# Kernel tuning notes

Hardware: AMD Instinct MI355X
Metric: run time of the kernel (lower is better)

Reference implementation:

```python
import jax, jax.numpy as jnp
import numpy as np

N_HEAD, MODEL_DIM, KEY_DIM, VALUE_DIM = 16, 1024, 64, 64
B, S = 4, 2048
EPS = 1e-5
TEMP = float(np.sqrt(KEY_DIM))


def setup_inputs() -> dict:
    key = jax.random.key(0)
    ks = jax.random.split(key, 12)
    d = {
        'query': jax.random.normal(ks[0], (B, S, MODEL_DIM), jnp.float32),
        'key':   jax.random.normal(ks[1], (B, S, MODEL_DIM), jnp.float32),
        'value': jax.random.normal(ks[2], (B, S, MODEL_DIM), jnp.float32),
        # projection weights stored as [in, out]
        'Wq': jax.random.normal(ks[3], (MODEL_DIM, N_HEAD * KEY_DIM), jnp.float32) * np.sqrt(2.0 / (MODEL_DIM + KEY_DIM)),
        'bq': jnp.zeros((N_HEAD * KEY_DIM,), jnp.float32),
        'Wk': jax.random.normal(ks[4], (MODEL_DIM, N_HEAD * KEY_DIM), jnp.float32) * np.sqrt(2.0 / (MODEL_DIM + KEY_DIM)),
        'bk': jnp.zeros((N_HEAD * KEY_DIM,), jnp.float32),
        'Wv': jax.random.normal(ks[5], (MODEL_DIM, N_HEAD * VALUE_DIM), jnp.float32) * np.sqrt(2.0 / (MODEL_DIM + VALUE_DIM)),
        'bv': jnp.zeros((N_HEAD * VALUE_DIM,), jnp.float32),
        'Wo': jax.random.normal(ks[6], (N_HEAD * VALUE_DIM, MODEL_DIM), jnp.float32) * np.sqrt(2.0 / (N_HEAD * VALUE_DIM + MODEL_DIM)),
        'bo': jnp.zeros((MODEL_DIM,), jnp.float32),
        'ln_gamma': jnp.ones((MODEL_DIM,), jnp.float32),
        'ln_beta': jnp.zeros((MODEL_DIM,), jnp.float32),
    }
    return d


def reference(query, key, value, Wq, bq, Wk, bk, Wv, bv, Wo, bo, ln_gamma, ln_beta):
    b, sq, _ = query.shape
    residual = query
    # QKV projections -> [B, S, H, D]
    q = (query @ Wq + bq).reshape(b, sq, N_HEAD, KEY_DIM)
    k = (key @ Wk + bk).reshape(b, key.shape[1], N_HEAD, KEY_DIM)
    v = (value @ Wv + bv).reshape(b, value.shape[1], N_HEAD, VALUE_DIM)
    # scaled dot-product attention (dropout inactive in eval)
    scores = jnp.einsum('bqhd,bkhd->bhqk', q, k) / TEMP
    attn = jax.nn.softmax(scores, axis=-1)
    out = jnp.einsum('bhqk,bkhd->bqhd', attn, v).reshape(b, sq, N_HEAD * VALUE_DIM)
    # output projection + residual + LayerNorm
    out = out @ Wo + bo + residual
    mu = jnp.mean(out, axis=-1, keepdims=True)
    var = jnp.var(out, axis=-1, keepdims=True)
    return (out - mu) * jax.lax.rsqrt(var + EPS) * ln_gamma + ln_beta
```

## Files before the change

### kernel.cpp

```cpp
#include <hip/hip_runtime.h>
#include <math.h>

#define MD 1024
#define NH 16
#define HD 64
#define BATCH 4
#define SEQ 2048

typedef __attribute__((ext_vector_type(8))) short short8;
typedef __attribute__((ext_vector_type(4))) short short4v;
typedef __attribute__((ext_vector_type(4))) float f32x4;
typedef __attribute__((ext_vector_type(2))) unsigned int uint2v;

#define GLOAD16(gp, lp) __builtin_amdgcn_global_load_lds( \
    (const __attribute__((address_space(1))) void*)(gp),  \
    (__attribute__((address_space(3))) void*)(lp), 16, 0, 0)

__device__ inline unsigned short f2b(float f) {
    unsigned u = __builtin_bit_cast(unsigned, f);
    unsigned r = (u + 0x7fffu + ((u >> 16) & 1u)) >> 16;
    return (unsigned short)r;
}
__device__ inline float b2f(unsigned short s) {
    return __builtin_bit_cast(float, ((unsigned)s) << 16);
}

__global__ __launch_bounds__(256)
void prep_kernel(const float* __restrict__ x0, const float* __restrict__ x1,
                 const float* __restrict__ x2, unsigned short* __restrict__ y0,
                 unsigned short* __restrict__ y1, unsigned short* __restrict__ y2,
                 int n,
                 const float* __restrict__ W0, const float* __restrict__ W1,
                 const float* __restrict__ W2, const float* __restrict__ W3,
                 unsigned short* __restrict__ T0, unsigned short* __restrict__ T1,
                 unsigned short* __restrict__ T2, unsigned short* __restrict__ T3)
{
    __shared__ __attribute__((aligned(16))) float T[64][68];
    const int tid = threadIdx.x;
    if (blockIdx.y < 3) {
        const float* x = (blockIdx.y == 0) ? x0 : (blockIdx.y == 1) ? x1 : x2;
        unsigned short* y = (blockIdx.y == 0) ? y0 : (blockIdx.y == 1) ? y1 : y2;
        int i = (blockIdx.x * 256 + tid) * 8;
        if (i >= n) return;
        f32x4 a = *(const f32x4*)(x + i);
        f32x4 b = *(const f32x4*)(x + i + 4);
        short8 o;
        o[0] = (short)f2b(a[0]); o[1] = (short)f2b(a[1]);
        o[2] = (short)f2b(a[2]); o[3] = (short)f2b(a[3]);
        o[4] = (short)f2b(b[0]); o[5] = (short)f2b(b[1]);
        o[6] = (short)f2b(b[2]); o[7] = (short)f2b(b[3]);
        *(short8*)(y + i) = o;
        return;
    }
    const int bx = blockIdx.x;
    if (bx >= 1024) return;
    const int z = bx >> 8, t = bx & 255;
    const int nt = t & 15, kt = t >> 4;
    const float* W = (z == 0) ? W0 : (z == 1) ? W1 : (z == 2) ? W2 : W3;
    unsigned short* WT = (z == 0) ? T0 : (z == 1) ? T1 : (z == 2) ? T2 : T3;
    #pragma unroll
    for (int i = 0; i < 4; ++i) {
        int u = tid + i * 256;
        int row = u >> 4, c4 = u & 15;
        f32x4 v = *(const f32x4*)(W + (size_t)(kt * 64 + row) * MD + nt * 64 + c4 * 4);
        *(f32x4*)&T[row][c4 * 4] = v;
    }
    __syncthreads();
    #pragma unroll
    for (int i = 0; i < 2; ++i) {
        int u = tid + i * 256;
        int nn = u >> 3, c16 = u & 7;
        short8 o;
        #pragma unroll
        for (int j = 0; j < 8; ++j) o[j] = (short)f2b(T[c16 * 8 + j][nn]);
        *(short8*)(WT + (size_t)(nt * 64 + nn) * MD + kt * 64 + c16 * 8) = o;
    }
}

__global__ __launch_bounds__(256)
void vtrans(const unsigned short* __restrict__ vp, unsigned short* __restrict__ vt)
{
    __shared__ __attribute__((aligned(16))) short T[64][72];
    const int tid = threadIdx.x;
    const int st = blockIdx.x, bh = blockIdx.y;
    const int b = bh >> 4, h = bh & 15;
    #pragma unroll
    for (int i = 0; i < 2; ++i) {
        int u = tid + i * 256;
        int row = u >> 3, c16 = u & 7;
        short8 v = *(const short8*)(vp + ((size_t)b * SEQ + st * 64 + row) * MD + h * 64 + c16 * 8);
        *(short8*)&T[row][c16 * 8] = v;
    }
    __syncthreads();
    #pragma unroll
    for (int i = 0; i < 2; ++i) {
        int u = tid + i * 256;
        int d = u >> 3, c16 = u & 7;
        short8 o;
        #pragma unroll
        for (int j = 0; j < 8; ++j) o[j] = T[c16 * 8 + j][d];
        *(short8*)(vt + ((size_t)bh * 64 + d) * SEQ + st * 64 + c16 * 8) = o;
    }
}

__device__ __forceinline__
void gemm_body(const unsigned short* __restrict__ A,
               const unsigned short* __restrict__ Bt,
               const float* __restrict__ bias,
               const float* __restrict__ residual,
               unsigned short* __restrict__ Cb,
               float* __restrict__ Cf,
               short* As, short* Bs)
{
    const int tid = threadIdx.x;
    const int lane = tid & 63;
    const int wave = tid >> 6;
    const int wm = wave >> 1, wn = wave & 1;
    const int l15 = lane & 15, g = lane >> 4;

    const int nbx = gridDim.x;
    const int bid = blockIdx.y * nbx + blockIdx.x;
    const int cpx = (nbx * gridDim.y) >> 3;
    const int swz = (bid & 7) * cpx + (bid >> 3);
    const int brow = (swz / nbx) * 128;
    const int bcol = (swz % nbx) * 128;

    f32x4 acc[4][4];
    #pragma unroll
    for (int m = 0; m < 4; ++m)
        #pragma unroll
        for (int n = 0; n < 4; ++n) acc[m][n] = (f32x4){0.f, 0.f, 0.f, 0.f};

    for (int k0 = 0; k0 < MD; k0 += 64) {
        __syncthreads();
        #pragma unroll
        for (int i = 0; i < 4; ++i) {
            const int U = (i * 4 + wave) * 64 + lane;
            const int row = U >> 3, c16 = U & 7;
            GLOAD16(A  + (size_t)(brow + row) * MD + k0 + c16 * 8, &As[U * 8]);
            GLOAD16(Bt + (size_t)(bcol + row) * MD + k0 + c16 * 8, &Bs[U * 8]);
        }
        __syncthreads();
        #pragma unroll
        for (int kk = 0; kk < 64; kk += 32) {
            short8 af[4], bf_[4];
            #pragma unroll
            for (int m = 0; m < 4; ++m)
                af[m] = *(const short8*)&As[(wm * 64 + m * 16 + l15) * 64 + kk + g * 8];
            #pragma unroll
            for (int n = 0; n < 4; ++n)
                bf_[n] = *(const short8*)&Bs[(wn * 64 + n * 16 + l15) * 64 + kk + g * 8];
            #pragma unroll
            for (int m = 0; m < 4; ++m)
                #pragma unroll
                for (int n = 0; n < 4; ++n)
                    acc[m][n] = __builtin_amdgcn_mfma_f32_16x16x32_bf16(af[m], bf_[n], acc[m][n], 0, 0, 0);
        }
    }

    #pragma unroll
    for (int m = 0; m < 4; ++m) {
        #pragma unroll
        for (int n = 0; n < 4; ++n) {
            const int col = bcol + wn * 64 + n * 16 + l15;
            const float bcol_v = bias[col];
            #pragma unroll
            for (int r = 0; r < 4; ++r) {
                const size_t row = (size_t)(brow + wm * 64 + m * 16 + 4 * g + r);
                float v = acc[m][n][r] + bcol_v;
                if (residual) v += residual[row * MD + col];
                if (Cb) Cb[row * MD + col] = f2b(v);
                else    Cf[row * MD + col] = v;
            }
        }
    }
}

__global__ __launch_bounds__(256, 2)
void gemm_qkv(const unsigned short* __restrict__ A0, const unsigned short* __restrict__ A1,
              const unsigned short* __restrict__ A2,
              const unsigned short* __restrict__ B0, const unsigned short* __restrict__ B1,
              const unsigned short* __restrict__ B2,
              const float* __restrict__ b0, const float* __restrict__ b1,
              const float* __restrict__ b2,
              unsigned short* __restrict__ C0, unsigned short* __restrict__ C1,
              unsigned short* __restrict__ C2)
{
    __shared__ __attribute__((aligned(16))) short As[128 * 64];
    __shared__ __attribute__((aligned(16))) short Bs[128 * 64];
    const int z = blockIdx.z;
    const unsigned short* A  = (z == 0) ? A0 : (z == 1) ? A1 : A2;
    const unsigned short* Bt = (z == 0) ? B0 : (z == 1) ? B1 : B2;
    const float* bias        = (z == 0) ? b0 : (z == 1) ? b1 : b2;
    unsigned short* C        = (z == 0) ? C0 : (z == 1) ? C1 : C2;
    gemm_body(A, Bt, bias, nullptr, C, nullptr, As, Bs);
}

__global__ __launch_bounds__(256, 2)
void gemm_o(const unsigned short* __restrict__ A, const unsigned short* __restrict__ Bt,
            const float* __restrict__ bias, const float* __restrict__ residual,
            float* __restrict__ Cf)
{
    __shared__ __attribute__((aligned(16))) short As[128 * 64];
    __shared__ __attribute__((aligned(16))) short Bs[128 * 64];
    gemm_body(A, Bt, bias, residual, nullptr, Cf, As, Bs);
}

__global__ __launch_bounds__(256, 2)
void attn_mfma(const unsigned short* __restrict__ qp,
               const unsigned short* __restrict__ kp,
               const unsigned short* __restrict__ vt,
               unsigned short* __restrict__ ao)
{
    __shared__ __attribute__((aligned(16))) short QPs[128 * 64];
    __shared__ __attribute__((aligned(16))) short Ks[2][64 * 64];
    __shared__ __attribute__((aligned(16))) short Vts[2][64 * 64];

    const int tid = threadIdx.x;
    const int lane = tid & 63;
    const int wave = tid >> 6;
    const int l15 = lane & 15, g = lane >> 4;
    const int qt = blockIdx.x, bh = blockIdx.y;
    const int b = bh >> 4, h = bh & 15;
    const size_t rowbase = (size_t)b * SEQ;
    const int q0 = qt * 128;
    const int wq = wave * 32;
    const int NT = SEQ / 64;

    const int r0 = tid >> 3, c16 = tid & 7;
    const int r1 = (tid + 256) >> 3;
    const int lds0 = (r0 * 8 + (c16 ^ (r0 & 7))) * 8;
    const int lds1 = (r1 * 8 + (c16 ^ (r1 & 7))) * 8;
    const unsigned short* kbase = kp + (rowbase + r0) * MD + h * 64 + c16 * 8;
    const unsigned short* vbase = vt + ((size_t)bh * 64 + r0) * SEQ + c16 * 8;

    const float qscale = 0.125f * 1.44269504088896f;
    #pragma unroll
    for (int i = 0; i < 4; ++i) {
        int u = tid + i * 256;
        int row = u >> 3, cc = u & 7;
        short8 v = *(const short8*)(qp + (rowbase + q0 + row) * MD + h * 64 + cc * 8);
        short8 o;
        #pragma unroll
        for (int j = 0; j < 8; ++j)
            o[j] = (short)f2b(b2f((unsigned short)v[j]) * qscale);
        *(short8*)&QPs[(row * 8 + (cc ^ (row & 7))) * 8] = o;
    }

    {
        short8 k0v = *(const short8*)(kbase);
        short8 k1v = *(const short8*)(kbase + 32 * MD);
        short8 v0v = *(const short8*)(vbase);
        short8 v1v = *(const short8*)(vbase + 32 * SEQ);
        *(short8*)&Ks[0][lds0]  = k0v;
        *(short8*)&Ks[0][lds1]  = k1v;
        *(short8*)&Vts[0][lds0] = v0v;
        *(short8*)&Vts[0][lds1] = v1v;
    }
    __syncthreads();

    short8 qreg[2][2];
    #pragma unroll
    for (int nf = 0; nf < 2; ++nf)
        #pragma unroll
        for (int ki = 0; ki < 2; ++ki) {
            int row = wq + nf * 16 + l15;
            int cu = ki * 4 + g;
            qreg[nf][ki] = *(const short8*)&QPs[(row * 8 + (cu ^ (row & 7))) * 8];
        }

    short8 ones;
    #pragma unroll
    for (int j = 0; j < 8; ++j) ones[j] = (short)0x3F80;

    float mrun[2] = {-INFINITY, -INFINITY};
    f32x4 lrun[2];
    f32x4 off[2][4];
    #pragma unroll
    for (int qf = 0; qf < 2; ++qf) {
        lrun[qf] = (f32x4){0.f, 0.f, 0.f, 0.f};
        #pragma unroll
        for (int df = 0; df < 4; ++df) off[qf][df] = (f32x4){0.f, 0.f, 0.f, 0.f};
    }

    for (int kt = 0; kt < NT; ++kt) {
        const int cur = kt & 1;

        short8 kreg0, kreg1, vreg0, vreg1;
        if (kt + 1 < NT) {
            const unsigned short* kb = kbase + (size_t)(kt + 1) * 64 * MD;
            const unsigned short* vb = vbase + (kt + 1) * 64;
            kreg0 = *(const short8*)(kb);
            kreg1 = *(const short8*)(kb + 32 * MD);
            vreg0 = *(const short8*)(vb);
            vreg1 = *(const short8*)(vb + 32 * SEQ);
        }

        f32x4 sc[4][2];
        #pragma unroll
        for (int mf = 0; mf < 4; ++mf)
            #pragma unroll
            for (int nf = 0; nf < 2; ++nf) sc[mf][nf] = (f32x4){0.f, 0.f, 0.f, 0.f};
        __builtin_amdgcn_s_setprio(1);
        #pragma unroll
        for (int ki = 0; ki < 2; ++ki) {
            const int cu = ki * 4 + g;
            short8 af[4];
            #pragma unroll
            for (int mf = 0; mf < 4; ++mf) {
                int row = mf * 16 + l15;
                af[mf] = *(const short8*)&Ks[cur][(row * 8 + (cu ^ (row & 7))) * 8];
            }
            #pragma unroll
            for (int mf = 0; mf < 4; ++mf)
                #pragma unroll
                for (int nf = 0; nf < 2; ++nf)
                    sc[mf][nf] = __builtin_amdgcn_mfma_f32_16x16x32_bf16(af[mf], qreg[nf][ki], sc[mf][nf], 0, 0, 0);
        }
        __builtin_amdgcn_s_setprio(0);

        float pmax[2];
        #pragma unroll
        for (int nf = 0; nf < 2; ++nf) {
            float pm = -INFINITY;
            #pragma unroll
            for (int mf = 0; mf < 4; ++mf)
                #pragma unroll
                for (int r = 0; r < 4; ++r) pm = fmaxf(pm, sc[mf][nf][r]);
            pm = fmaxf(pm, __shfl_xor(pm, 16));
            pm = fmaxf(pm, __shfl_xor(pm, 32));
            pmax[nf] = pm;
        }
        const int defer = (pmax[0] <= mrun[0] + 8.0f) && (pmax[1] <= mrun[1] + 8.0f);
        if (!__all(defer)) {
            float corr[2];
            #pragma unroll
            for (int nf = 0; nf < 2; ++nf) {
                float mnew = fmaxf(mrun[nf], pmax[nf]);
                corr[nf] = __builtin_amdgcn_exp2f(mrun[nf] - mnew);
                mrun[nf] = mnew;
            }
            #pragma unroll
            for (int qf = 0; qf < 2; ++qf)
                #pragma unroll
                for (int r = 0; r < 4; ++r) {
                    float c = __shfl(corr[qf], 4 * g + r);
                    lrun[qf][r] *= c;
                    #pragma unroll
                    for (int df = 0; df < 4; ++df) off[qf][df][r] *= c;
                }
        }
        #pragma unroll
        for (int nf = 0; nf < 2; ++nf) {
            const float nm = mrun[nf];
            #pragma unroll
            for (int mf = 0; mf < 4; ++mf)
                #pragma unroll
                for (int r = 0; r < 4; ++r)
                    sc[mf][nf][r] = __builtin_amdgcn_exp2f(sc[mf][nf][r] - nm);
        }

        #pragma unroll
        for (int nf = 0; nf < 2; ++nf) {
            int row = wq + nf * 16 + l15;
            #pragma unroll
            for (int mf = 0; mf < 4; ++mf) {
                unsigned p01, p23;
                asm("v_cvt_pk_bf16_f32 %0, %1, %2" : "=v"(p01) : "v"(sc[mf][nf][0]), "v"(sc[mf][nf][1]));
                asm("v_cvt_pk_bf16_f32 %0, %1, %2" : "=v"(p23) : "v"(sc[mf][nf][2]), "v"(sc[mf][nf][3]));
                uint2v pk = {p01, p23};
                int su = (mf * 2 + (g >> 1)) ^ (row & 7);
                *(uint2v*)&QPs[row * 64 + su * 8 + (g & 1) * 4] = pk;
            }
        }

        f32x4 ts[2];
        ts[0] = (f32x4){0.f, 0.f, 0.f, 0.f};
        ts[1] = (f32x4){0.f, 0.f, 0.f, 0.f};
        __builtin_amdgcn_s_setprio(1);
        #pragma unroll
        for (int ki = 0; ki < 2; ++ki) {
            const int cu = ki * 4 + g;
            short8 pa[2], vb[4];
            #pragma unroll
            for (int qf = 0; qf < 2; ++qf) {
                int row = wq + qf * 16 + l15;
                pa[qf] = *(const short8*)&QPs[(row * 8 + (cu ^ (row & 7))) * 8];
            }
            #pragma unroll
            for (int df = 0; df < 4; ++df) {
                int d = df * 16 + l15;
                vb[df] = *(const short8*)&Vts[cur][(d * 8 + (cu ^ (d & 7))) * 8];
            }
            #pragma unroll
            for (int qf = 0; qf < 2; ++qf)
                #pragma unroll
                for (int df = 0; df < 4; ++df)
                    off[qf][df] = __builtin_amdgcn_mfma_f32_16x16x32_bf16(pa[qf], vb[df], off[qf][df], 0, 0, 0);
            #pragma unroll
            for (int qf = 0; qf < 2; ++qf)
                ts[qf] = __builtin_amdgcn_mfma_f32_16x16x32_bf16(pa[qf], ones, ts[qf], 0, 0, 0);
        }
        __builtin_amdgcn_s_setprio(0);
        #pragma unroll
        for (int qf = 0; qf < 2; ++qf)
            #pragma unroll
            for (int r = 0; r < 4; ++r) lrun[qf][r] += ts[qf][r];

        if (kt + 1 < NT) {
            const int nxt = cur ^ 1;
            *(short8*)&Ks[nxt][lds0]  = kreg0;
            *(short8*)&Ks[nxt][lds1]  = kreg1;
            *(short8*)&Vts[nxt][lds0] = vreg0;
            *(short8*)&Vts[nxt][lds1] = vreg1;
        }
        __syncthreads();
    }

    #pragma unroll
    for (int qf = 0; qf < 2; ++qf) {
        #pragma unroll
        for (int r = 0; r < 4; ++r) {
            const float inv = 1.0f / lrun[qf][r];
            const size_t row = rowbase + q0 + wq + qf * 16 + 4 * g + r;
            #pragma unroll
            for (int df = 0; df < 4; ++df) {
                float val = off[qf][df][r] * inv;
                ao[row * MD + h * 64 + df * 16 + l15] = f2b(val);
            }
        }
    }
}

__global__ __launch_bounds__(256)
void ln_kernel(float* __restrict__ X, const float* __restrict__ gamma,
               const float* __restrict__ beta)
{
    const int row = blockIdx.x;
    const int tid = threadIdx.x;
    float* px = X + (size_t)row * MD;
    f32x4 x = ((const f32x4*)px)[tid];
    float s  = x[0] + x[1] + x[2] + x[3];
    float ss = fmaf(x[0], x[0], fmaf(x[1], x[1], fmaf(x[2], x[2], x[3] * x[3])));
    #pragma unroll
    for (int off = 1; off < 64; off <<= 1) {
        s  += __shfl_xor(s,  off);
        ss += __shfl_xor(ss, off);
    }
    __shared__ float red[8];
    const int wid = tid >> 6;
    if ((tid & 63) == 0) { red[wid] = s; red[wid + 4] = ss; }
    __syncthreads();
    s  = red[0] + red[1] + red[2] + red[3];
    ss = red[4] + red[5] + red[6] + red[7];
    const float mu   = s * (1.0f / MD);
    const float var  = ss * (1.0f / MD) - mu * mu;
    const float rstd = rsqrtf(var + 1e-5f);
    f32x4 gm = ((const f32x4*)gamma)[tid];
    f32x4 be = ((const f32x4*)beta)[tid];
    f32x4 r;
    r[0] = (x[0] - mu) * rstd * gm[0] + be[0];
    r[1] = (x[1] - mu) * rstd * gm[1] + be[1];
    r[2] = (x[2] - mu) * rstd * gm[2] + be[2];
    r[3] = (x[3] - mu) * rstd * gm[3] + be[3];
    ((f32x4*)px)[tid] = r;
}

extern "C" void kernel_launch(void* const* d_in, const int* in_sizes, int n_in,
                              void* d_out, int out_size, void* d_ws, size_t ws_size,
                              hipStream_t stream)
{
    const float* query = (const float*)d_in[0];
    const float* key   = (const float*)d_in[1];
    const float* value = (const float*)d_in[2];
    const float* Wq = (const float*)d_in[3];
    const float* bq = (const float*)d_in[4];
    const float* Wk = (const float*)d_in[5];
    const float* bk = (const float*)d_in[6];
    const float* Wv = (const float*)d_in[7];
    const float* bv = (const float*)d_in[8];
    const float* Wo = (const float*)d_in[9];
    const float* bo = (const float*)d_in[10];
    const float* gamma = (const float*)d_in[11];
    const float* beta  = (const float*)d_in[12];
    float* out = (float*)d_out;

    const size_t NTOK = (size_t)BATCH * SEQ;
    const size_t ACT  = NTOK * MD;

    unsigned short* qa  = (unsigned short*)d_ws;
    unsigned short* ka  = qa + ACT;
    unsigned short* va  = ka + ACT;
    unsigned short* WqT = va + ACT;
    unsigned short* WkT = WqT + (size_t)MD * MD;
    unsigned short* WvT = WkT + (size_t)MD * MD;
    unsigned short* WoT = WvT + (size_t)MD * MD;
    unsigned short* qp  = WoT + (size_t)MD * MD;
    unsigned short* kp  = qp + ACT;
    unsigned short* vp  = kp + ACT;
    unsigned short* vtb = qa;
    unsigned short* ao  = ka;

    dim3 blk(256);

    prep_kernel<<<dim3(4096, 4), blk, 0, stream>>>(
        query, key, value, qa, ka, va, (int)ACT,
        Wq, Wk, Wv, Wo, WqT, WkT, WvT, WoT);

    dim3 gg(MD / 128, NTOK / 128, 3);
    gemm_qkv<<<gg, blk, 0, stream>>>(qa, ka, va, WqT, WkT, WvT,
                                     bq, bk, bv, qp, kp, vp);

    vtrans<<<dim3(SEQ / 64, 64), blk, 0, stream>>>(vp, vtb);

    attn_mfma<<<dim3(SEQ / 128, 64), blk, 0, stream>>>(qp, kp, vtb, ao);

    gemm_o<<<dim3(MD / 128, NTOK / 128), blk, 0, stream>>>(ao, WoT, bo, query, out);

    ln_kernel<<<NTOK, blk, 0, stream>>>(out, gamma, beta);
}
```

Measured before the change: 248.9 us.

## Fuse V transpose and Q scaling into QKV GEMM epilogue; widen attention tiles

The QKV GEMM epilogue now writes V directly in transposed per-head layout, which removes the separate vtrans kernel. It also folds the softmax scale (1/sqrt(d)·log2e) into Q, so attention loads Q fragments straight from global memory into registers instead of staging them through LDS. The attention kernel now processes 256 queries per block (64 per wave), doubling K/V reuse and halving the grid. The trade-off is higher register pressure (more accumulators and score tiles), a larger P buffer in LDS, and only 512 attention blocks, which may lower occupancy.

```diff
diff --git a/kernel.cpp b/kernel.cpp
--- a/kernel.cpp
+++ b/kernel.cpp
@@ -77,40 +77,11 @@
     }
 }
 
-__global__ __launch_bounds__(256)
-void vtrans(const unsigned short* __restrict__ vp, unsigned short* __restrict__ vt)
-{
-    __shared__ __attribute__((aligned(16))) short T[64][72];
-    const int tid = threadIdx.x;
-    const int st = blockIdx.x, bh = blockIdx.y;
-    const int b = bh >> 4, h = bh & 15;
-    #pragma unroll
-    for (int i = 0; i < 2; ++i) {
-        int u = tid + i * 256;
-        int row = u >> 3, c16 = u & 7;
-        short8 v = *(const short8*)(vp + ((size_t)b * SEQ + st * 64 + row) * MD + h * 64 + c16 * 8);
-        *(short8*)&T[row][c16 * 8] = v;
-    }
-    __syncthreads();
-    #pragma unroll
-    for (int i = 0; i < 2; ++i) {
-        int u = tid + i * 256;
-        int d = u >> 3, c16 = u & 7;
-        short8 o;
-        #pragma unroll
-        for (int j = 0; j < 8; ++j) o[j] = T[c16 * 8 + j][d];
-        *(short8*)(vt + ((size_t)bh * 64 + d) * SEQ + st * 64 + c16 * 8) = o;
-    }
-}
-
 __device__ __forceinline__
-void gemm_body(const unsigned short* __restrict__ A,
+void gemm_core(const unsigned short* __restrict__ A,
                const unsigned short* __restrict__ Bt,
-               const float* __restrict__ bias,
-               const float* __restrict__ residual,
-               unsigned short* __restrict__ Cb,
-               float* __restrict__ Cf,
-               short* As, short* Bs)
+               short* As, short* Bs, f32x4 acc[4][4],
+               int* obrow, int* obcol)
 {
     const int tid = threadIdx.x;
     const int lane = tid & 63;
@@ -124,8 +95,8 @@
     const int swz = (bid & 7) * cpx + (bid >> 3);
     const int brow = (swz / nbx) * 128;
     const int bcol = (swz % nbx) * 128;
-
-    f32x4 acc[4][4];
+    *obrow = brow; *obcol = bcol;
+
     #pragma unroll
     for (int m = 0; m < 4; ++m)
         #pragma unroll
@@ -155,23 +126,6 @@
                 #pragma unroll
                 for (int n = 0; n < 4; ++n)
                     acc[m][n] = __builtin_amdgcn_mfma_f32_16x16x32_bf16(af[m], bf_[n], acc[m][n], 0, 0, 0);
-        }
-    }
-
-    #pragma unroll
-    for (int m = 0; m < 4; ++m) {
-        #pragma unroll
-        for (int n = 0; n < 4; ++n) {
-            const int col = bcol + wn * 64 + n * 16 + l15;
-            const float bcol_v = bias[col];
-            #pragma unroll
-            for (int r = 0; r < 4; ++r) {
-                const size_t row = (size_t)(brow + wm * 64 + m * 16 + 4 * g + r);
-                float v = acc[m][n][r] + bcol_v;
-                if (residual) v += residual[row * MD + col];
-                if (Cb) Cb[row * MD + col] = f2b(v);
-                else    Cf[row * MD + col] = v;
-            }
         }
     }
 }
@@ -183,8 +137,8 @@
               const unsigned short* __restrict__ B2,
               const float* __restrict__ b0, const float* __restrict__ b1,
               const float* __restrict__ b2,
-              unsigned short* __restrict__ C0, unsigned short* __restrict__ C1,
-              unsigned short* __restrict__ C2)
+              unsigned short* __restrict__ Cq, unsigned short* __restrict__ Ck,
+              unsigned short* __restrict__ Cvt)
 {
     __shared__ __attribute__((aligned(16))) short As[128 * 64];
     __shared__ __attribute__((aligned(16))) short Bs[128 * 64];
@@ -192,8 +146,50 @@
     const unsigned short* A  = (z == 0) ? A0 : (z == 1) ? A1 : A2;
     const unsigned short* Bt = (z == 0) ? B0 : (z == 1) ? B1 : B2;
     const float* bias        = (z == 0) ? b0 : (z == 1) ? b1 : b2;
-    unsigned short* C        = (z == 0) ? C0 : (z == 1) ? C1 : C2;
-    gemm_body(A, Bt, bias, nullptr, C, nullptr, As, Bs);
+
+    f32x4 acc[4][4];
+    int brow, bcol;
+    gemm_core(A, Bt, As, Bs, acc, &brow, &bcol);
+
+    const int tid = threadIdx.x;
+    const int lane = tid & 63;
+    const int wave = tid >> 6;
+    const int wm = wave >> 1, wn = wave & 1;
+    const int l15 = lane & 15, g = lane >> 4;
+
+    if (z == 2) {
+        #pragma unroll
+        for (int m = 0; m < 4; ++m) {
+            #pragma unroll
+            for (int n = 0; n < 4; ++n) {
+                const int col = bcol + wn * 64 + n * 16 + l15;
+                const int h = col >> 6, d = col & 63;
+                const float bv_ = bias[col];
+                const int row0 = brow + wm * 64 + m * 16 + 4 * g;
+                const int bb = row0 >> 11, s = row0 & 2047;
+                short4v pk;
+                #pragma unroll
+                for (int r = 0; r < 4; ++r) pk[r] = (short)f2b(acc[m][n][r] + bv_);
+                *(short4v*)(Cvt + ((size_t)((bb << 4) + h) * 64 + d) * SEQ + s) = pk;
+            }
+        }
+        return;
+    }
+    const float scale = (z == 0) ? (0.125f * 1.44269504088896f) : 1.0f;
+    unsigned short* C = (z == 0) ? Cq : Ck;
+    #pragma unroll
+    for (int m = 0; m < 4; ++m) {
+        #pragma unroll
+        for (int n = 0; n < 4; ++n) {
+            const int col = bcol + wn * 64 + n * 16 + l15;
+            const float bcol_v = bias[col];
+            #pragma unroll
+            for (int r = 0; r < 4; ++r) {
+                const size_t row = (size_t)(brow + wm * 64 + m * 16 + 4 * g + r);
+                C[row * MD + col] = f2b((acc[m][n][r] + bcol_v) * scale);
+            }
+        }
+    }
 }
 
 __global__ __launch_bounds__(256, 2)
@@ -203,7 +199,28 @@
 {
     __shared__ __attribute__((aligned(16))) short As[128 * 64];
     __shared__ __attribute__((aligned(16))) short Bs[128 * 64];
-    gemm_body(A, Bt, bias, residual, nullptr, Cf, As, Bs);
+    f32x4 acc[4][4];
+    int brow, bcol;
+    gemm_core(A, Bt, As, Bs, acc, &brow, &bcol);
+
+    const int tid = threadIdx.x;
+    const int lane = tid & 63;
+    const int wave = tid >> 6;
+    const int wm = wave >> 1, wn = wave & 1;
+    const int l15 = lane & 15, g = lane >> 4;
+    #pragma unroll
+    for (int m = 0; m < 4; ++m) {
+        #pragma unroll
+        for (int n = 0; n < 4; ++n) {
+            const int col = bcol + wn * 64 + n * 16 + l15;
+            const float bcol_v = bias[col];
+            #pragma unroll
+            for (int r = 0; r < 4; ++r) {
+                const size_t row = (size_t)(brow + wm * 64 + m * 16 + 4 * g + r);
+                Cf[row * MD + col] = acc[m][n][r] + bcol_v + residual[row * MD + col];
+            }
+        }
+    }
 }
 
 __global__ __launch_bounds__(256, 2)
@@ -212,7 +229,7 @@
                const unsigned short* __restrict__ vt,
                unsigned short* __restrict__ ao)
 {
-    __shared__ __attribute__((aligned(16))) short QPs[128 * 64];
+    __shared__ __attribute__((aligned(16))) short Ps[256 * 64];
     __shared__ __attribute__((aligned(16))) short Ks[2][64 * 64];
     __shared__ __attribute__((aligned(16))) short Vts[2][64 * 64];
 
@@ -223,29 +240,24 @@
     const int qt = blockIdx.x, bh = blockIdx.y;
     const int b = bh >> 4, h = bh & 15;
     const size_t rowbase = (size_t)b * SEQ;
-    const int q0 = qt * 128;
-    const int wq = wave * 32;
+    const int q0 = qt * 256;
+    const int wq = wave * 64;
     const int NT = SEQ / 64;
 
     const int r0 = tid >> 3, c16 = tid & 7;
-    const int r1 = (tid + 256) >> 3;
+    const int r1 = r0 + 32;
     const int lds0 = (r0 * 8 + (c16 ^ (r0 & 7))) * 8;
     const int lds1 = (r1 * 8 + (c16 ^ (r1 & 7))) * 8;
     const unsigned short* kbase = kp + (rowbase + r0) * MD + h * 64 + c16 * 8;
     const unsigned short* vbase = vt + ((size_t)bh * 64 + r0) * SEQ + c16 * 8;
 
-    const float qscale = 0.125f * 1.44269504088896f;
-    #pragma unroll
-    for (int i = 0; i < 4; ++i) {
-        int u = tid + i * 256;
-        int row = u >> 3, cc = u & 7;
-        short8 v = *(const short8*)(qp + (rowbase + q0 + row) * MD + h * 64 + cc * 8);
-        short8 o;
-        #pragma unroll
-        for (int j = 0; j < 8; ++j)
-            o[j] = (short)f2b(b2f((unsigned short)v[j]) * qscale);
-        *(short8*)&QPs[(row * 8 + (cc ^ (row & 7))) * 8] = o;
-    }
+    short8 qreg[4][2];
+    #pragma unroll
+    for (int nf = 0; nf < 4; ++nf)
+        #pragma unroll
+        for (int ki = 0; ki < 2; ++ki)
+            qreg[nf][ki] = *(const short8*)(qp + (rowbase + q0 + wq + nf * 16 + l15) * MD
+                                               + h * 64 + ki * 32 + g * 8);
 
     {
         short8 k0v = *(const short8*)(kbase);
@@ -259,25 +271,15 @@
     }
     __syncthreads();
 
-    short8 qreg[2][2];
-    #pragma unroll
-    for (int nf = 0; nf < 2; ++nf)
-        #pragma unroll
-        for (int ki = 0; ki < 2; ++ki) {
-            int row = wq + nf * 16 + l15;
-            int cu = ki * 4 + g;
-            qreg[nf][ki] = *(const short8*)&QPs[(row * 8 + (cu ^ (row & 7))) * 8];
-        }
-
     short8 ones;
     #pragma unroll
     for (int j = 0; j < 8; ++j) ones[j] = (short)0x3F80;
 
-    float mrun[2] = {-INFINITY, -INFINITY};
-    f32x4 lrun[2];
-    f32x4 off[2][4];
-    #pragma unroll
-    for (int qf = 0; qf < 2; ++qf) {
+    float mrun[4] = {-INFINITY, -INFINITY, -INFINITY, -INFINITY};
+    f32x4 lrun[4];
+    f32x4 off[4][4];
+    #pragma unroll
+    for (int qf = 0; qf < 4; ++qf) {
         lrun[qf] = (f32x4){0.f, 0.f, 0.f, 0.f};
         #pragma unroll
         for (int df = 0; df < 4; ++df) off[qf][df] = (f32x4){0.f, 0.f, 0.f, 0.f};
@@ -296,11 +298,11 @@
             vreg1 = *(const short8*)(vb + 32 * SEQ);
         }
 
-        f32x4 sc[4][2];
+        f32x4 sc[4][4];
         #pragma unroll
         for (int mf = 0; mf < 4; ++mf)
             #pragma unroll
-            for (int nf = 0; nf < 2; ++nf) sc[mf][nf] = (f32x4){0.f, 0.f, 0.f, 0.f};
+            for (int nf = 0; nf < 4; ++nf) sc[mf][nf] = (f32x4){0.f, 0.f, 0.f, 0.f};
         __builtin_amdgcn_s_setprio(1);
         #pragma unroll
         for (int ki = 0; ki < 2; ++ki) {
@@ -314,14 +316,14 @@
             #pragma unroll
             for (int mf = 0; mf < 4; ++mf)
                 #pragma unroll
-                for (int nf = 0; nf < 2; ++nf)
+                for (int nf = 0; nf < 4; ++nf)
                     sc[mf][nf] = __builtin_amdgcn_mfma_f32_16x16x32_bf16(af[mf], qreg[nf][ki], sc[mf][nf], 0, 0, 0);
         }
         __builtin_amdgcn_s_setprio(0);
 
-        float pmax[2];
-        #pragma unroll
-        for (int nf = 0; nf < 2; ++nf) {
+        float pmax[4];
+        #pragma unroll
+        for (int nf = 0; nf < 4; ++nf) {
             float pm = -INFINITY;
             #pragma unroll
             for (int mf = 0; mf < 4; ++mf)
@@ -331,17 +333,18 @@
             pm = fmaxf(pm, __shfl_xor(pm, 32));
             pmax[nf] = pm;
         }
-        const int defer = (pmax[0] <= mrun[0] + 8.0f) && (pmax[1] <= mrun[1] + 8.0f);
+        const int defer = (pmax[0] <= mrun[0] + 8.0f) && (pmax[1] <= mrun[1] + 8.0f) &&
+                          (pmax[2] <= mrun[2] + 8.0f) && (pmax[3] <= mrun[3] + 8.0f);
         if (!__all(defer)) {
-            float corr[2];
-            #pragma unroll
-            for (int nf = 0; nf < 2; ++nf) {
+            float corr[4];
+            #pragma unroll
+            for (int nf = 0; nf < 4; ++nf) {
                 float mnew = fmaxf(mrun[nf], pmax[nf]);
                 corr[nf] = __builtin_amdgcn_exp2f(mrun[nf] - mnew);
                 mrun[nf] = mnew;
             }
             #pragma unroll
-            for (int qf = 0; qf < 2; ++qf)
+            for (int qf = 0; qf < 4; ++qf)
                 #pragma unroll
                 for (int r = 0; r < 4; ++r) {
                     float c = __shfl(corr[qf], 4 * g + r);
@@ -351,7 +354,7 @@
                 }
         }
         #pragma unroll
-        for (int nf = 0; nf < 2; ++nf) {
+        for (int nf = 0; nf < 4; ++nf) {
             const float nm = mrun[nf];
             #pragma unroll
             for (int mf = 0; mf < 4; ++mf)
@@ -361,7 +364,7 @@
         }
 
         #pragma unroll
-        for (int nf = 0; nf < 2; ++nf) {
+        for (int nf = 0; nf < 4; ++nf) {
             int row = wq + nf * 16 + l15;
             #pragma unroll
             for (int mf = 0; mf < 4; ++mf) {
@@ -370,22 +373,22 @@
                 asm("v_cvt_pk_bf16_f32 %0, %1, %2" : "=v"(p23) : "v"(sc[mf][nf][2]), "v"(sc[mf][nf][3]));
                 uint2v pk = {p01, p23};
                 int su = (mf * 2 + (g >> 1)) ^ (row & 7);
-                *(uint2v*)&QPs[row * 64 + su * 8 + (g & 1) * 4] = pk;
-            }
-        }
-
-        f32x4 ts[2];
-        ts[0] = (f32x4){0.f, 0.f, 0.f, 0.f};
-        ts[1] = (f32x4){0.f, 0.f, 0.f, 0.f};
+                *(uint2v*)&Ps[row * 64 + su * 8 + (g & 1) * 4] = pk;
+            }
+        }
+
+        f32x4 ts[4];
+        #pragma unroll
+        for (int qf = 0; qf < 4; ++qf) ts[qf] = (f32x4){0.f, 0.f, 0.f, 0.f};
         __builtin_amdgcn_s_setprio(1);
         #pragma unroll
         for (int ki = 0; ki < 2; ++ki) {
             const int cu = ki * 4 + g;
-            short8 pa[2], vb[4];
-            #pragma unroll
-            for (int qf = 0; qf < 2; ++qf) {
+            short8 pa[4], vb[4];
+            #pragma unroll
+            for (int qf = 0; qf < 4; ++qf) {
                 int row = wq + qf * 16 + l15;
-                pa[qf] = *(const short8*)&QPs[(row * 8 + (cu ^ (row & 7))) * 8];
+                pa[qf] = *(const short8*)&Ps[(row * 8 + (cu ^ (row & 7))) * 8];
             }
             #pragma unroll
             for (int df = 0; df < 4; ++df) {
@@ -393,17 +396,17 @@
                 vb[df] = *(const short8*)&Vts[cur][(d * 8 + (cu ^ (d & 7))) * 8];
             }
             #pragma unroll
-            for (int qf = 0; qf < 2; ++qf)
+            for (int qf = 0; qf < 4; ++qf)
                 #pragma unroll
                 for (int df = 0; df < 4; ++df)
                     off[qf][df] = __builtin_amdgcn_mfma_f32_16x16x32_bf16(pa[qf], vb[df], off[qf][df], 0, 0, 0);
             #pragma unroll
-            for (int qf = 0; qf < 2; ++qf)
+            for (int qf = 0; qf < 4; ++qf)
                 ts[qf] = __builtin_amdgcn_mfma_f32_16x16x32_bf16(pa[qf], ones, ts[qf], 0, 0, 0);
         }
         __builtin_amdgcn_s_setprio(0);
         #pragma unroll
-        for (int qf = 0; qf < 2; ++qf)
+        for (int qf = 0; qf < 4; ++qf)
             #pragma unroll
             for (int r = 0; r < 4; ++r) lrun[qf][r] += ts[qf][r];
 
@@ -418,7 +421,7 @@
     }
 
     #pragma unroll
-    for (int qf = 0; qf < 2; ++qf) {
+    for (int qf = 0; qf < 4; ++qf) {
         #pragma unroll
         for (int r = 0; r < 4; ++r) {
             const float inv = 1.0f / lrun[qf][r];
@@ -497,8 +500,7 @@
     unsigned short* WoT = WvT + (size_t)MD * MD;
     unsigned short* qp  = WoT + (size_t)MD * MD;
     unsigned short* kp  = qp + ACT;
-    unsigned short* vp  = kp + ACT;
-    unsigned short* vtb = qa;
+    unsigned short* vtp = kp + ACT;
     unsigned short* ao  = ka;
 
     dim3 blk(256);
@@ -509,11 +511,9 @@
 
     dim3 gg(MD / 128, NTOK / 128, 3);
     gemm_qkv<<<gg, blk, 0, stream>>>(qa, ka, va, WqT, WkT, WvT,
-                                     bq, bk, bv, qp, kp, vp);
-
-    vtrans<<<dim3(SEQ / 64, 64), blk, 0, stream>>>(vp, vtb);
-
-    attn_mfma<<<dim3(SEQ / 128, 64), blk, 0, stream>>>(qp, kp, vtb, ao);
+                                     bq, bk, bv, qp, kp, vtp);
+
+    attn_mfma<<<dim3(SEQ / 256, 64), blk, 0, stream>>>(qp, kp, vtp, ao);
 
     gemm_o<<<dim3(MD / 128, NTOK / 128), blk, 0, stream>>>(ao, WoT, bo, query, out);
 
```

New measurement: 225.1 us. -9.6%, faster.
